# Performance work log

Hardware: AMD Instinct MI355X
Metric: run time of the kernel (lower is better)

The kernel has to match this reference:

```python
import jax, jax.numpy as jnp
import numpy as np


def log_g(x):
    # log of g(x) = where(x>=0, x+0.5, sigmoid(x))
    return jnp.where(x >= 0, jnp.log(jax.nn.relu(x) + 0.5), -jax.nn.softplus(-x))


def setup_inputs() -> dict:
    key = jax.random.key(0)
    ks = jax.random.split(key, 6)
    B, S, D, Din = 4, 4096, 1024, 2048
    x = jax.random.normal(ks[0], (B, S, D), jnp.float32)
    s1 = 1.0 / np.sqrt(D)
    W1 = jax.random.normal(ks[1], (D, 3 * Din), jnp.float32) * s1
    b1 = jax.random.normal(ks[2], (3 * Din,), jnp.float32) * s1
    b1 = b1.at[Din:2 * Din].add(1.0)  # forget_bias_init_scale = 1.0
    s2 = 1.0 / np.sqrt(Din)
    W2 = jax.random.normal(ks[3], (Din, D), jnp.float32) * s2
    b2 = jax.random.normal(ks[4], (D,), jnp.float32) * s2
    init_h = jax.random.normal(ks[5], (Din,), jnp.float32)
    return {"x": x, "W1": W1, "b1": b1, "W2": W2, "b2": b2, "init_h": init_h}


def reference(x, W1, b1, W2, b2, init_h):
    B, S, _ = x.shape
    Din = init_h.shape[0]
    proj = x @ W1 + b1                              # [B,S,3*Din]
    hidden, forget_gate, input_gate = jnp.split(proj, 3, axis=-1)
    # use_coeff_norm = True branch (normalized gates in log space)
    diff = jax.nn.softplus(-forget_gate) - jax.nn.softplus(-input_gate)
    log_coeffs = -jax.nn.softplus(diff)             # log(f/(f+i))
    log_val_coeffs = -jax.nn.softplus(-diff)        # log(i/(f+i))
    log_values = log_val_coeffs + log_g(hidden)     # [B,S,Din]
    # prepend learned initial hidden state
    prev_log_hidden = jnp.broadcast_to(log_g(init_h), (B, 1, Din))
    log_values = jnp.concatenate([prev_log_hidden, log_values], axis=1)  # [B,S+1,Din]
    log_coeffs = jnp.pad(log_coeffs, ((0, 0), (1, 0), (0, 0)))           # [B,S+1,Din]
    # heinsen associative scan in log space
    a_star = jnp.cumsum(log_coeffs, axis=1)
    log_h = a_star + jax.lax.cumlogsumexp(log_values - a_star, axis=1)
    out_h = jnp.exp(log_h[:, -S:])                  # [B,S,Din]
    next_hidden = out_h[:, -1:]
    next_log_hidden = log_h[:, -1:]
    out = out_h @ W2 + b2                           # [B,S,D]
    return (out, next_hidden, next_log_hidden)
```

## Files before the change

kernel.cpp:

```cpp
#include <hip/hip_runtime.h>
#include <cstdint>
#include <cstddef>

#define BB 4
#define SS 4096
#define DD 1024
#define DIN 2048
#define MTOT (BB*SS)
#define K1 DD
#define K2 DIN
#define N2 DD
#define NCH (BB*DIN)
#define NCHUNK 32
#define CLEN (SS/NCHUNK)

typedef _Float16 half8  __attribute__((ext_vector_type(8)));
typedef _Float16 half4v __attribute__((ext_vector_type(4)));
typedef float    floatx4 __attribute__((ext_vector_type(4)));

#define AS1(p) ((__attribute__((address_space(1))) void*)(uintptr_t)(p))
#define AS3(p) ((__attribute__((address_space(3))) void*)(uint32_t)(uintptr_t)(p))

__device__ __forceinline__ void gload16(const void* g, void* l) {
  __builtin_amdgcn_global_load_lds(AS1(g), AS3(l), 16, 0, 0);
}

__device__ __forceinline__ float sigm(float x) { return 1.f / (1.f + __expf(-x)); }
__device__ __forceinline__ uint32_t hbits(float f) {
  _Float16 h = (_Float16)f; uint16_t u; __builtin_memcpy(&u, &h, 2); return (uint32_t)u;
}
__device__ __forceinline__ float h_lo(uint32_t v) {
  uint16_t u = (uint16_t)(v & 0xffffu); _Float16 h; __builtin_memcpy(&h, &u, 2); return (float)h;
}
__device__ __forceinline__ float h_hi(uint32_t v) {
  uint16_t u = (uint16_t)(v >> 16); _Float16 h; __builtin_memcpy(&h, &u, 2); return (float)h;
}


__global__ void f32_to_f16_vec(const float* __restrict__ src, _Float16* __restrict__ dst) {
  int i = (blockIdx.x * blockDim.x + threadIdx.x) * 4;
  float4 v = *(const float4*)(src + i);
  half4v o; o.x = (_Float16)v.x; o.y = (_Float16)v.y; o.z = (_Float16)v.z; o.w = (_Float16)v.w;
  *(half4v*)(dst + i) = o;
}

__global__ void transpose_cvt(const float* __restrict__ src, _Float16* __restrict__ dst,
                              int R, int C) {
  __shared__ float t[32][33];
  int c0 = blockIdx.x * 32, r0 = blockIdx.y * 32;
  int tx = threadIdx.x, ty = threadIdx.y;
#pragma unroll
  for (int j = 0; j < 32; j += 8)
    t[ty + j][tx] = src[(size_t)(r0 + ty + j) * C + c0 + tx];
  __syncthreads();
#pragma unroll
  for (int j = 0; j < 32; j += 8)
    dst[(size_t)(c0 + ty + j) * R + r0 + tx] = (_Float16)t[tx][ty + j];
}

__global__ __launch_bounds__(256) void gemm1_fused(
    const _Float16* __restrict__ xh, const _Float16* __restrict__ w1t,
    const float* __restrict__ b1, uint32_t* __restrict__ zg) {
  __shared__ _Float16 As[128 * 32];
  __shared__ _Float16 Bs[3][64 * 32];

  const int tid = threadIdx.x;
  const int wave = tid >> 6, lane = tid & 63;
  const int wm = wave >> 1, wn = wave & 1;
  const int m0 = blockIdx.y * 128;
  const int d0 = blockIdx.x * 64;
  const int lrow = lane >> 2;
  const int lk = (((lane & 3) ^ (lrow & 3)) * 8);
  const int roff = ((((lane & 15) << 2) | ((lane >> 4) ^ (lane & 3))) * 8);

  floatx4 acc[3][4][2] = {};

  for (int k0 = 0; k0 < K1; k0 += 32) {
    __syncthreads();
#pragma unroll
    for (int i = 0; i < 2; ++i) {
      int chunk = wave * 2 + i;
      gload16(xh + (size_t)(m0 + chunk * 16 + lrow) * K1 + k0 + lk, As + chunk * 512);
    }
#pragma unroll
    for (int gt = 0; gt < 3; ++gt)
      gload16(w1t + (size_t)(gt * DIN + d0 + wave * 16 + lrow) * K1 + k0 + lk,
              &Bs[gt][wave * 512]);
    asm volatile("s_waitcnt vmcnt(0)" ::: "memory");
    __syncthreads();

    half8 af[4], bfr[3][2];
#pragma unroll
    for (int mi = 0; mi < 4; ++mi)
      af[mi] = *(const half8*)(As + (wm * 4 + mi) * 512 + roff);
#pragma unroll
    for (int gt = 0; gt < 3; ++gt)
#pragma unroll
      for (int ni = 0; ni < 2; ++ni)
        bfr[gt][ni] = *(const half8*)(&Bs[gt][(wn * 2 + ni) * 512 + roff]);
#pragma unroll
    for (int gt = 0; gt < 3; ++gt)
#pragma unroll
      for (int mi = 0; mi < 4; ++mi)
#pragma unroll
        for (int ni = 0; ni < 2; ++ni)
          acc[gt][mi][ni] = __builtin_amdgcn_mfma_f32_16x16x32_f16(
              af[mi], bfr[gt][ni], acc[gt][mi][ni], 0, 0, 0);
  }

#pragma unroll
  for (int ni = 0; ni < 2; ++ni) {
    int d = d0 + wn * 32 + ni * 16 + (lane & 15);
    float bh = b1[d], bf_ = b1[DIN + d], bi = b1[2 * DIN + d];
#pragma unroll
    for (int mi = 0; mi < 4; ++mi) {
#pragma unroll
      for (int r = 0; r < 4; ++r) {
        int m = m0 + wm * 64 + mi * 16 + (lane >> 4) * 4 + r;
        float hv = acc[0][mi][ni][r] + bh;
        float fv = acc[1][mi][ni][r] + bf_;
        float iv = acc[2][mi][ni][r] + bi;
        float u = 1.f + __expf(-fminf(fmaxf(fv, -30.f), 30.f));
        float v = 1.f + __expf(-fminf(fmaxf(iv, -30.f), 30.f));
        float z = __fdividef(u, u + v);
        float gg = (hv >= 0.f) ? (hv + 0.5f)
                               : __fdividef(1.f, 1.f + __expf(-fmaxf(hv, -30.f)));
        zg[(size_t)m * DIN + d] = hbits(z) | (hbits(gg) << 16);
      }
    }
  }
}


__global__ void scanA(const uint32_t* __restrict__ zg,
                      float* __restrict__ cA, float* __restrict__ cB) {
  int gidx = blockIdx.x * 256 + threadIdx.x;
  int q = gidx >> 13, c = gidx & (NCH - 1);
  int b = c >> 11, d = c & (DIN - 1);
  size_t base = ((size_t)b * SS + q * CLEN) * DIN + d;
  float A = 1.f, Bv = 0.f;
#pragma unroll 4
  for (int t = 0; t < CLEN; ++t) {
    uint32_t v = zg[base + (size_t)t * DIN];
    float z = h_lo(v), g = h_hi(v);
    A *= (1.f - z);
    Bv = fmaf(z, g - Bv, Bv);
  }
  cA[q * NCH + c] = A;
  cB[q * NCH + c] = Bv;
}

__global__ void scanB(const float* __restrict__ cA, const float* __restrict__ cB,
                      const float* __restrict__ init_h, float* __restrict__ cH) {
  int c = blockIdx.x * 256 + threadIdx.x;
  int d = c & (DIN - 1);
  float x = init_h[d];
  float h = (x >= 0.f) ? (x + 0.5f) : sigm(x);
#pragma unroll
  for (int q = 0; q < NCHUNK; ++q) {
    cH[q * NCH + c] = h;
    h = fmaf(cA[q * NCH + c], h, cB[q * NCH + c]);
  }
}

__global__ void scanC(const uint32_t* __restrict__ zg, const float* __restrict__ cH,
                      _Float16* __restrict__ hh, float* __restrict__ out_tail) {
  int gidx = blockIdx.x * 256 + threadIdx.x;
  int q = gidx >> 13, c = gidx & (NCH - 1);
  int b = c >> 11, d = c & (DIN - 1);
  size_t base = ((size_t)b * SS + q * CLEN) * DIN + d;
  float h = cH[q * NCH + c];
#pragma unroll 4
  for (int t = 0; t < CLEN; ++t) {
    uint32_t v = zg[base + (size_t)t * DIN];
    float z = h_lo(v), g = h_hi(v);
    h = fmaf(z, g - h, h);
    hh[base + (size_t)t * DIN] = (_Float16)h;
  }
  if (q == NCHUNK - 1) {
    out_tail[c] = h;
    out_tail[NCH + c] = logf(h);
  }
}

__global__ __launch_bounds__(256) void gemm2k(
    const _Float16* __restrict__ hh, const _Float16* __restrict__ w2t,
    const float* __restrict__ b2, float* __restrict__ out) {
  __shared__ _Float16 As[128 * 32];
  __shared__ _Float16 Bs[128 * 32];

  const int tid = threadIdx.x;
  const int wave = tid >> 6, lane = tid & 63;
  const int wm = wave >> 1, wn = wave & 1;
  const int m0 = blockIdx.y * 128;
  const int n0 = blockIdx.x * 128;
  const int lrow = lane >> 2;
  const int lk = (((lane & 3) ^ (lrow & 3)) * 8);
  const int roff = ((((lane & 15) << 2) | ((lane >> 4) ^ (lane & 3))) * 8);

  floatx4 acc[4][4] = {};

  for (int k0 = 0; k0 < K2; k0 += 32) {
    __syncthreads();
#pragma unroll
    for (int i = 0; i < 2; ++i) {
      int chunk = wave * 2 + i;
      gload16(hh  + (size_t)(m0 + chunk * 16 + lrow) * K2 + k0 + lk, As + chunk * 512);
      gload16(w2t + (size_t)(n0 + chunk * 16 + lrow) * K2 + k0 + lk, Bs + chunk * 512);
    }
    asm volatile("s_waitcnt vmcnt(0)" ::: "memory");
    __syncthreads();

    half8 af[4], bfr[4];
#pragma unroll
    for (int mi = 0; mi < 4; ++mi)
      af[mi] = *(const half8*)(As + (wm * 4 + mi) * 512 + roff);
#pragma unroll
    for (int ni = 0; ni < 4; ++ni)
      bfr[ni] = *(const half8*)(Bs + (wn * 4 + ni) * 512 + roff);
#pragma unroll
    for (int mi = 0; mi < 4; ++mi)
#pragma unroll
      for (int ni = 0; ni < 4; ++ni)
        acc[mi][ni] = __builtin_amdgcn_mfma_f32_16x16x32_f16(af[mi], bfr[ni], acc[mi][ni], 0, 0, 0);
  }

#pragma unroll
  for (int ni = 0; ni < 4; ++ni) {
    int n = n0 + wn * 64 + ni * 16 + (lane & 15);
    float bias = b2[n];
#pragma unroll
    for (int mi = 0; mi < 4; ++mi) {
#pragma unroll
      for (int r = 0; r < 4; ++r) {
        int m = m0 + wm * 64 + mi * 16 + (lane >> 4) * 4 + r;
        out[(size_t)m * N2 + n] = acc[mi][ni][r] + bias;
      }
    }
  }
}


extern "C" void kernel_launch(void* const* d_in, const int* in_sizes, int n_in,
                              void* d_out, int out_size, void* d_ws, size_t ws_size,
                              hipStream_t stream) {
  const float* x      = (const float*)d_in[0];
  const float* W1     = (const float*)d_in[1];
  const float* b1     = (const float*)d_in[2];
  const float* W2     = (const float*)d_in[3];
  const float* b2     = (const float*)d_in[4];
  const float* init_h = (const float*)d_in[5];
  float* out = (float*)d_out;

  char* w = (char*)d_ws;
  _Float16* xh  = (_Float16*)w; w += (size_t)MTOT * K1 * 2;
  _Float16* w1t = (_Float16*)w; w += (size_t)3 * DIN * K1 * 2;
  _Float16* w2t = (_Float16*)w; w += (size_t)N2 * K2 * 2;
  uint32_t* zg  = (uint32_t*)w; w += (size_t)MTOT * DIN * 4;
  _Float16* hh  = (_Float16*)w; w += (size_t)MTOT * DIN * 2;
  float* cA = (float*)w; w += (size_t)NCH * NCHUNK * 4;
  float* cB = (float*)w; w += (size_t)NCH * NCHUNK * 4;
  float* cH = (float*)w; w += (size_t)NCH * NCHUNK * 4;

  f32_to_f16_vec<<<dim3(MTOT * K1 / 1024), dim3(256), 0, stream>>>(x, xh);
  transpose_cvt<<<dim3(3 * DIN / 32, K1 / 32), dim3(32, 8), 0, stream>>>(W1, w1t, K1, 3 * DIN);
  transpose_cvt<<<dim3(N2 / 32, K2 / 32), dim3(32, 8), 0, stream>>>(W2, w2t, K2, N2);

  gemm1_fused<<<dim3(DIN / 64, MTOT / 128), dim3(256), 0, stream>>>(xh, w1t, b1, zg);

  scanA<<<dim3(NCH * NCHUNK / 256), dim3(256), 0, stream>>>(zg, cA, cB);
  scanB<<<dim3(NCH / 256), dim3(256), 0, stream>>>(cA, cB, init_h, cH);
  scanC<<<dim3(NCH * NCHUNK / 256), dim3(256), 0, stream>>>(zg, cH, hh, out + (size_t)MTOT * DD);

  gemm2k<<<dim3(N2 / 128, MTOT / 128), dim3(256), 0, stream>>>(hh, w2t, b2, out);
}
```

Measured before the change: 594.0 us.

## Double-buffer LDS tiles in both GEMM kernels to overlap loads with MFMA

Both GEMM kernels now keep two LDS buffers. Each iteration issues the global-to-LDS loads for the next K-slice before running the MFMA work on the current slice, with one barrier per iteration instead of two. The aim is to hide global memory latency behind the matrix math. In exchange LDS use doubles, which may lower occupancy. The explicit vmcnt wait is gone, so the code relies on the barrier's implicit wait to make the asynchronous LDS writes visible.

```diff
diff --git a/kernel.cpp b/kernel.cpp
--- a/kernel.cpp
+++ b/kernel.cpp
@@ -61,8 +61,8 @@
 __global__ __launch_bounds__(256) void gemm1_fused(
     const _Float16* __restrict__ xh, const _Float16* __restrict__ w1t,
     const float* __restrict__ b1, uint32_t* __restrict__ zg) {
-  __shared__ _Float16 As[128 * 32];
-  __shared__ _Float16 Bs[3][64 * 32];
+  __shared__ _Float16 As[2][128 * 32];
+  __shared__ _Float16 Bs[2][3][64 * 32];
 
   const int tid = threadIdx.x;
   const int wave = tid >> 6, lane = tid & 63;
@@ -75,29 +75,36 @@
 
   floatx4 acc[3][4][2] = {};
 
-  for (int k0 = 0; k0 < K1; k0 += 32) {
-    __syncthreads();
-#pragma unroll
-    for (int i = 0; i < 2; ++i) {
-      int chunk = wave * 2 + i;
-      gload16(xh + (size_t)(m0 + chunk * 16 + lrow) * K1 + k0 + lk, As + chunk * 512);
-    }
+#define STAGE1(bf, k0)                                                           \
+  do {                                                                           \
+    _Pragma("unroll")                                                            \
+    for (int i = 0; i < 2; ++i) {                                                \
+      int chunk = wave * 2 + i;                                                  \
+      gload16(xh + (size_t)(m0 + chunk * 16 + lrow) * K1 + (k0) + lk,            \
+              &As[bf][chunk * 512]);                                             \
+    }                                                                            \
+    _Pragma("unroll")                                                            \
+    for (int gt = 0; gt < 3; ++gt)                                               \
+      gload16(w1t + (size_t)(gt * DIN + d0 + wave * 16 + lrow) * K1 + (k0) + lk, \
+              &Bs[bf][gt][wave * 512]);                                          \
+  } while (0)
+
+  STAGE1(0, 0);
+  __syncthreads();
+
+  for (int it = 0; it < K1 / 32; ++it) {
+    const int cur = it & 1;
+    if (it + 1 < K1 / 32) STAGE1(cur ^ 1, (it + 1) * 32);
+
+    half8 af[4], bfr[3][2];
+#pragma unroll
+    for (int mi = 0; mi < 4; ++mi)
+      af[mi] = *(const half8*)(&As[cur][(wm * 4 + mi) * 512 + roff]);
 #pragma unroll
     for (int gt = 0; gt < 3; ++gt)
-      gload16(w1t + (size_t)(gt * DIN + d0 + wave * 16 + lrow) * K1 + k0 + lk,
-              &Bs[gt][wave * 512]);
-    asm volatile("s_waitcnt vmcnt(0)" ::: "memory");
-    __syncthreads();
-
-    half8 af[4], bfr[3][2];
-#pragma unroll
-    for (int mi = 0; mi < 4; ++mi)
-      af[mi] = *(const half8*)(As + (wm * 4 + mi) * 512 + roff);
-#pragma unroll
-    for (int gt = 0; gt < 3; ++gt)
 #pragma unroll
       for (int ni = 0; ni < 2; ++ni)
-        bfr[gt][ni] = *(const half8*)(&Bs[gt][(wn * 2 + ni) * 512 + roff]);
+        bfr[gt][ni] = *(const half8*)(&Bs[cur][gt][(wn * 2 + ni) * 512 + roff]);
 #pragma unroll
     for (int gt = 0; gt < 3; ++gt)
 #pragma unroll
@@ -106,7 +113,9 @@
         for (int ni = 0; ni < 2; ++ni)
           acc[gt][mi][ni] = __builtin_amdgcn_mfma_f32_16x16x32_f16(
               af[mi], bfr[gt][ni], acc[gt][mi][ni], 0, 0, 0);
-  }
+    __syncthreads();
+  }
+#undef STAGE1
 
 #pragma unroll
   for (int ni = 0; ni < 2; ++ni) {
@@ -186,8 +195,8 @@
 __global__ __launch_bounds__(256) void gemm2k(
     const _Float16* __restrict__ hh, const _Float16* __restrict__ w2t,
     const float* __restrict__ b2, float* __restrict__ out) {
-  __shared__ _Float16 As[128 * 32];
-  __shared__ _Float16 Bs[128 * 32];
+  __shared__ _Float16 As[2][128 * 32];
+  __shared__ _Float16 Bs[2][128 * 32];
 
   const int tid = threadIdx.x;
   const int wave = tid >> 6, lane = tid & 63;
@@ -200,30 +209,40 @@
 
   floatx4 acc[4][4] = {};
 
-  for (int k0 = 0; k0 < K2; k0 += 32) {
-    __syncthreads();
-#pragma unroll
-    for (int i = 0; i < 2; ++i) {
-      int chunk = wave * 2 + i;
-      gload16(hh  + (size_t)(m0 + chunk * 16 + lrow) * K2 + k0 + lk, As + chunk * 512);
-      gload16(w2t + (size_t)(n0 + chunk * 16 + lrow) * K2 + k0 + lk, Bs + chunk * 512);
-    }
-    asm volatile("s_waitcnt vmcnt(0)" ::: "memory");
-    __syncthreads();
+#define STAGE2(bf, k0)                                                          \
+  do {                                                                          \
+    _Pragma("unroll")                                                           \
+    for (int i = 0; i < 2; ++i) {                                               \
+      int chunk = wave * 2 + i;                                                 \
+      gload16(hh  + (size_t)(m0 + chunk * 16 + lrow) * K2 + (k0) + lk,          \
+              &As[bf][chunk * 512]);                                            \
+      gload16(w2t + (size_t)(n0 + chunk * 16 + lrow) * K2 + (k0) + lk,          \
+              &Bs[bf][chunk * 512]);                                            \
+    }                                                                           \
+  } while (0)
+
+  STAGE2(0, 0);
+  __syncthreads();
+
+  for (int it = 0; it < K2 / 32; ++it) {
+    const int cur = it & 1;
+    if (it + 1 < K2 / 32) STAGE2(cur ^ 1, (it + 1) * 32);
 
     half8 af[4], bfr[4];
 #pragma unroll
     for (int mi = 0; mi < 4; ++mi)
-      af[mi] = *(const half8*)(As + (wm * 4 + mi) * 512 + roff);
+      af[mi] = *(const half8*)(&As[cur][(wm * 4 + mi) * 512 + roff]);
 #pragma unroll
     for (int ni = 0; ni < 4; ++ni)
-      bfr[ni] = *(const half8*)(Bs + (wn * 4 + ni) * 512 + roff);
+      bfr[ni] = *(const half8*)(&Bs[cur][(wn * 4 + ni) * 512 + roff]);
 #pragma unroll
     for (int mi = 0; mi < 4; ++mi)
 #pragma unroll
       for (int ni = 0; ni < 4; ++ni)
         acc[mi][ni] = __builtin_amdgcn_mfma_f32_16x16x32_f16(af[mi], bfr[ni], acc[mi][ni], 0, 0, 0);
-  }
+    __syncthreads();
+  }
+#undef STAGE2
 
 #pragma unroll
   for (int ni = 0; ni < 4; ++ni) {
```

Measured after the change: 600.3 us. About the same (+1.1%).

## Pipeline both GEMM main loops with four-stage LDS ring buffers

Applied to the files above, without the earlier changes.

Both GEMM kernels replace the single LDS tile with a ring of four buffers. Global-to-LDS loads run two k-steps ahead, and a partial `vmcnt` wait plus a single barrier per step replaces the old full drain and double barrier. The aim is to overlap global memory latency with MFMA work and cut synchronisation stalls. In exchange, LDS use grows several-fold, which may lower occupancy, and the last prefetches read past the end of each row's K range.

```diff
diff --git a/kernel.cpp b/kernel.cpp
--- a/kernel.cpp
+++ b/kernel.cpp
@@ -61,8 +61,8 @@
 __global__ __launch_bounds__(256) void gemm1_fused(
     const _Float16* __restrict__ xh, const _Float16* __restrict__ w1t,
     const float* __restrict__ b1, uint32_t* __restrict__ zg) {
-  __shared__ _Float16 As[128 * 32];
-  __shared__ _Float16 Bs[3][64 * 32];
+  __shared__ _Float16 As[4][128 * 32];
+  __shared__ _Float16 Bs[4][3][64 * 32];
 
   const int tid = threadIdx.x;
   const int wave = tid >> 6, lane = tid & 63;
@@ -73,39 +73,57 @@
   const int lk = (((lane & 3) ^ (lrow & 3)) * 8);
   const int roff = ((((lane & 15) << 2) | ((lane >> 4) ^ (lane & 3))) * 8);
 
+  const _Float16* pA0 = xh + (size_t)(m0 + (wave * 2 + 0) * 16 + lrow) * K1 + lk;
+  const _Float16* pA1 = pA0 + (size_t)16 * K1;
+  const _Float16* pB0 = w1t + (size_t)(d0 + wave * 16 + lrow) * K1 + lk;
+  const _Float16* pB1 = pB0 + (size_t)DIN * K1;
+  const _Float16* pB2 = pB1 + (size_t)DIN * K1;
+
   floatx4 acc[3][4][2] = {};
 
-  for (int k0 = 0; k0 < K1; k0 += 32) {
-    __syncthreads();
-#pragma unroll
-    for (int i = 0; i < 2; ++i) {
-      int chunk = wave * 2 + i;
-      gload16(xh + (size_t)(m0 + chunk * 16 + lrow) * K1 + k0 + lk, As + chunk * 512);
+#pragma unroll
+  for (int t = 0; t < 2; ++t) {
+    gload16(pA0 + t * 32, &As[t][(wave * 2 + 0) * 512]);
+    gload16(pA1 + t * 32, &As[t][(wave * 2 + 1) * 512]);
+    gload16(pB0 + t * 32, &Bs[t][0][wave * 512]);
+    gload16(pB1 + t * 32, &Bs[t][1][wave * 512]);
+    gload16(pB2 + t * 32, &Bs[t][2][wave * 512]);
+  }
+  pA0 += 64; pA1 += 64; pB0 += 64; pB1 += 64; pB2 += 64;
+
+  for (int ito = 0; ito < K1 / 32 / 4; ++ito) {
+#pragma unroll
+    for (int ii = 0; ii < 4; ++ii) {
+      const int sb = (ii + 2) & 3, rb = ii;
+      gload16(pA0, &As[sb][(wave * 2 + 0) * 512]);
+      gload16(pA1, &As[sb][(wave * 2 + 1) * 512]);
+      gload16(pB0, &Bs[sb][0][wave * 512]);
+      gload16(pB1, &Bs[sb][1][wave * 512]);
+      gload16(pB2, &Bs[sb][2][wave * 512]);
+      pA0 += 32; pA1 += 32; pB0 += 32; pB1 += 32; pB2 += 32;
+
+      asm volatile("s_waitcnt vmcnt(10)" ::: "memory");
+      __builtin_amdgcn_s_barrier();
+      asm volatile("" ::: "memory");
+
+      half8 af[4], bfr[3][2];
+#pragma unroll
+      for (int mi = 0; mi < 4; ++mi)
+        af[mi] = *(const half8*)(&As[rb][(wm * 4 + mi) * 512 + roff]);
+#pragma unroll
+      for (int gt = 0; gt < 3; ++gt)
+#pragma unroll
+        for (int ni = 0; ni < 2; ++ni)
+          bfr[gt][ni] = *(const half8*)(&Bs[rb][gt][(wn * 2 + ni) * 512 + roff]);
+#pragma unroll
+      for (int gt = 0; gt < 3; ++gt)
+#pragma unroll
+        for (int mi = 0; mi < 4; ++mi)
+#pragma unroll
+          for (int ni = 0; ni < 2; ++ni)
+            acc[gt][mi][ni] = __builtin_amdgcn_mfma_f32_16x16x32_f16(
+                af[mi], bfr[gt][ni], acc[gt][mi][ni], 0, 0, 0);
     }
-#pragma unroll
-    for (int gt = 0; gt < 3; ++gt)
-      gload16(w1t + (size_t)(gt * DIN + d0 + wave * 16 + lrow) * K1 + k0 + lk,
-              &Bs[gt][wave * 512]);
-    asm volatile("s_waitcnt vmcnt(0)" ::: "memory");
-    __syncthreads();
-
-    half8 af[4], bfr[3][2];
-#pragma unroll
-    for (int mi = 0; mi < 4; ++mi)
-      af[mi] = *(const half8*)(As + (wm * 4 + mi) * 512 + roff);
-#pragma unroll
-    for (int gt = 0; gt < 3; ++gt)
-#pragma unroll
-      for (int ni = 0; ni < 2; ++ni)
-        bfr[gt][ni] = *(const half8*)(&Bs[gt][(wn * 2 + ni) * 512 + roff]);
-#pragma unroll
-    for (int gt = 0; gt < 3; ++gt)
-#pragma unroll
-      for (int mi = 0; mi < 4; ++mi)
-#pragma unroll
-        for (int ni = 0; ni < 2; ++ni)
-          acc[gt][mi][ni] = __builtin_amdgcn_mfma_f32_16x16x32_f16(
-              af[mi], bfr[gt][ni], acc[gt][mi][ni], 0, 0, 0);
   }
 
 #pragma unroll
@@ -186,8 +204,8 @@
 __global__ __launch_bounds__(256) void gemm2k(
     const _Float16* __restrict__ hh, const _Float16* __restrict__ w2t,
     const float* __restrict__ b2, float* __restrict__ out) {
-  __shared__ _Float16 As[128 * 32];
-  __shared__ _Float16 Bs[128 * 32];
+  __shared__ _Float16 As[4][128 * 32];
+  __shared__ _Float16 Bs[4][128 * 32];
 
   const int tid = threadIdx.x;
   const int wave = tid >> 6, lane = tid & 63;
@@ -198,31 +216,49 @@
   const int lk = (((lane & 3) ^ (lrow & 3)) * 8);
   const int roff = ((((lane & 15) << 2) | ((lane >> 4) ^ (lane & 3))) * 8);
 
+  const _Float16* pA0 = hh + (size_t)(m0 + (wave * 2 + 0) * 16 + lrow) * K2 + lk;
+  const _Float16* pA1 = pA0 + (size_t)16 * K2;
+  const _Float16* pB0 = w2t + (size_t)(n0 + (wave * 2 + 0) * 16 + lrow) * K2 + lk;
+  const _Float16* pB1 = pB0 + (size_t)16 * K2;
+
   floatx4 acc[4][4] = {};
 
-  for (int k0 = 0; k0 < K2; k0 += 32) {
-    __syncthreads();
-#pragma unroll
-    for (int i = 0; i < 2; ++i) {
-      int chunk = wave * 2 + i;
-      gload16(hh  + (size_t)(m0 + chunk * 16 + lrow) * K2 + k0 + lk, As + chunk * 512);
-      gload16(w2t + (size_t)(n0 + chunk * 16 + lrow) * K2 + k0 + lk, Bs + chunk * 512);
+#pragma unroll
+  for (int t = 0; t < 2; ++t) {
+    gload16(pA0 + t * 32, &As[t][(wave * 2 + 0) * 512]);
+    gload16(pA1 + t * 32, &As[t][(wave * 2 + 1) * 512]);
+    gload16(pB0 + t * 32, &Bs[t][(wave * 2 + 0) * 512]);
+    gload16(pB1 + t * 32, &Bs[t][(wave * 2 + 1) * 512]);
+  }
+  pA0 += 64; pA1 += 64; pB0 += 64; pB1 += 64;
+
+  for (int ito = 0; ito < K2 / 32 / 4; ++ito) {
+#pragma unroll
+    for (int ii = 0; ii < 4; ++ii) {
+      const int sb = (ii + 2) & 3, rb = ii;
+      gload16(pA0, &As[sb][(wave * 2 + 0) * 512]);
+      gload16(pA1, &As[sb][(wave * 2 + 1) * 512]);
+      gload16(pB0, &Bs[sb][(wave * 2 + 0) * 512]);
+      gload16(pB1, &Bs[sb][(wave * 2 + 1) * 512]);
+      pA0 += 32; pA1 += 32; pB0 += 32; pB1 += 32;
+
+      asm volatile("s_waitcnt vmcnt(8)" ::: "memory");
+      __builtin_amdgcn_s_barrier();
+      asm volatile("" ::: "memory");
+
+      half8 af[4], bfr[4];
+#pragma unroll
+      for (int mi = 0; mi < 4; ++mi)
+        af[mi] = *(const half8*)(&As[rb][(wm * 4 + mi) * 512 + roff]);
+#pragma unroll
+      for (int ni = 0; ni < 4; ++ni)
+        bfr[ni] = *(const half8*)(&Bs[rb][(wn * 4 + ni) * 512 + roff]);
+#pragma unroll
+      for (int mi = 0; mi < 4; ++mi)
+#pragma unroll
+        for (int ni = 0; ni < 4; ++ni)
+          acc[mi][ni] = __builtin_amdgcn_mfma_f32_16x16x32_f16(af[mi], bfr[ni], acc[mi][ni], 0, 0, 0);
     }
-    asm volatile("s_waitcnt vmcnt(0)" ::: "memory");
-    __syncthreads();
-
-    half8 af[4], bfr[4];
-#pragma unroll
-    for (int mi = 0; mi < 4; ++mi)
-      af[mi] = *(const half8*)(As + (wm * 4 + mi) * 512 + roff);
-#pragma unroll
-    for (int ni = 0; ni < 4; ++ni)
-      bfr[ni] = *(const half8*)(Bs + (wn * 4 + ni) * 512 + roff);
-#pragma unroll
-    for (int mi = 0; mi < 4; ++mi)
-#pragma unroll
-      for (int ni = 0; ni < 4; ++ni)
-        acc[mi][ni] = __builtin_amdgcn_mfma_f32_16x16x32_f16(af[mi], bfr[ni], acc[mi][ni], 0, 0, 0);
   }
 
 #pragma unroll
```

After: 588.2 us. About the same (-1.0%).
